# Kernel optimization log

Measured on AMD Instinct MI355X. Metric: run time of the kernel, lower is better.

Reference implementation:

```python
import jax, jax.numpy as jnp
import numpy as np
import math

N_ENTITIES = 200000
N_ITEMS = 100000
N_REL = 40
DIM = 64
N_HEADS = 2
DK = DIM // N_HEADS
N_EDGES = 1500000
K_EDGES = 256
K_ITEMS = 100


def setup_inputs() -> dict:
    key = jax.random.key(0)
    k1, k2, k3, k4, k5, k6 = jax.random.split(key, 6)
    entity_emb = jax.random.normal(k1, (N_ENTITIES, DIM), jnp.float32) * 0.1
    W_Q = jax.random.normal(k2, (DIM, DIM), jnp.float32) * (1.0 / math.sqrt(DIM))
    relation_emb = jax.random.normal(k3, (N_REL - 1, DIM), jnp.float32) * 0.1
    edge_index = jax.random.randint(k4, (2, N_EDGES), 0, N_ENTITIES, jnp.int32)
    # edge_type in [1, N_REL-1]: code indexes relation_emb[edge_type - 1]
    edge_type = jax.random.randint(k5, (N_EDGES,), 1, N_REL, jnp.int32)
    # uniform(0,1) driving the gumbel noise -log(-log(u)); clipped away from 0
    noise_u = jax.random.uniform(k6, (N_EDGES,), jnp.float32, 1e-9, 1.0)
    return {"entity_emb": entity_emb, "W_Q": W_Q, "relation_emb": relation_emb,
            "noise_u": noise_u, "edge_index": edge_index, "edge_type": edge_type}


def reference(entity_emb, W_Q, relation_emb, noise_u, edge_index, edge_type):
    head, tail = edge_index[0], edge_index[1]
    E = edge_index.shape[1]

    # --- norm_attn_computer (AttnHGCN): per-edge multi-head attention ---
    # project once on nodes, then gather (same math as (emb[head] @ W_Q))
    proj = entity_emb @ W_Q                               # [N, D]
    q = proj[head].reshape(E, N_HEADS, DK)                # [E, H, Dk]
    k = proj[tail].reshape(E, N_HEADS, DK)                # [E, H, Dk]
    rel = relation_emb[edge_type - 1].reshape(E, N_HEADS, DK)
    attn = jnp.sum(q * k * rel, axis=-1) / math.sqrt(DK)  # [E, H]
    edge_attn_logits = attn.mean(axis=-1)                 # [E]

    # scatter_softmax over head nodes, then multiply by head degree (norm)
    seg_max = jax.lax.stop_gradient(
        jax.ops.segment_max(edge_attn_logits, head, num_segments=N_ENTITIES))
    ex = jnp.exp(edge_attn_logits - seg_max[head])
    denom = jax.ops.segment_sum(ex, head, num_segments=N_ENTITIES)
    edge_attn_score = ex / denom[head]
    deg = jax.ops.segment_sum(jnp.ones_like(edge_attn_logits), head,
                              num_segments=N_ENTITIES)
    edge_attn_score = edge_attn_score * deg[head]         # [E]

    # --- attn logit sums per item (head + tail scatter_sum), topk 100 ---
    sum_by_node = (jax.ops.segment_sum(edge_attn_logits, head, num_segments=N_ENTITIES)
                   + jax.ops.segment_sum(edge_attn_logits, tail, num_segments=N_ENTITIES))
    top_items_v, top_attn_items = jax.lax.top_k(sum_by_node[:N_ITEMS], K_ITEMS)

    # --- gumbel-noise injection + edge topk 256 ---
    noisy_score = edge_attn_score + (-jnp.log(-jnp.log(noise_u)))
    topk_v, topk_attn_edge_id = jax.lax.top_k(noisy_score, K_EDGES)

    return (edge_attn_score, topk_v, topk_attn_edge_id, top_items_v, top_attn_items)
```

## Files before the change

### kernel.cpp

```cpp
#include <hip/hip_runtime.h>

#define N_ENTITIES 200000
#define N_ITEMS    100000
#define DIM        64
#define N_EDGES    1500000
#define K_EDGES    256
#define K_ITEMS    100
#define SCALE      0.08838834764831845f

#define CAND_CAP   8192
#define NSCANB     ((N_ENTITIES + 255) / 256)
#define NXCD       8
#define NBLK3      1024

typedef unsigned long long u64;


__device__ __forceinline__ void l2_atomic_add_f32(float* p, float v) {
    asm volatile("global_atomic_add_f32 %0, %1, off" :: "v"(p), "v"(v) : "memory");
}
__device__ __forceinline__ unsigned xcd_atomic_add(unsigned* p, unsigned v) {
    return __hip_atomic_fetch_add(p, v, __ATOMIC_RELAXED, __HIP_MEMORY_SCOPE_WORKGROUP);
}

__device__ __forceinline__ unsigned fkey(float x) {
    unsigned u = __float_as_uint(x);
    return (u & 0x80000000u) ? ~u : (u | 0x80000000u);
}
__device__ __forceinline__ float funkey(unsigned k) {
    return (k & 0x80000000u) ? __uint_as_float(k & 0x7fffffffu)
                             : __uint_as_float(~k);
}

__device__ __forceinline__ unsigned select_digit(const unsigned* __restrict__ hist,
                                                 unsigned Keff, unsigned* above) {
    unsigned cum = 0;
    int b = 255;
    for (; b > 0; --b) {
        unsigned hb = hist[b];
        if (cum + hb >= Keff) break;
        cum += hb;
    }
    *above = cum;
    return (unsigned)b;
}

__global__ __launch_bounds__(256) void proj_kernel(const float* __restrict__ emb,
                                                   const float* __restrict__ W,
                                                   float* __restrict__ proj,
                                                   const int* __restrict__ head,
                                                   unsigned* __restrict__ degiX,
                                                   unsigned* __restrict__ rank) {
    unsigned xcd;
    asm volatile("s_getreg_b32 %0, hwreg(HW_REG_XCC_ID)" : "=s"(xcd));
    xcd &= (NXCD - 1);

    int e = blockIdx.x * blockDim.x + threadIdx.x;
    unsigned rk = 0;
    bool haveEdge = (e < N_EDGES);
    if (haveEdge)
        rk = (xcd << 28) | xcd_atomic_add(&degiX[(size_t)xcd * N_ENTITIES + head[e]], 1u);

    __shared__ float part[4][16][64];
    const int t = threadIdx.x;
    const int c = t & 63;
    const int q = __builtin_amdgcn_readfirstlane(t >> 6);

    float Wreg[16];
#pragma unroll
    for (int j = 0; j < 16; ++j) Wreg[j] = W[(q * 16 + j) * 64 + c];

    const int base = blockIdx.x * 16;
    const float* erow = emb + (size_t)base * 64 + q * 16;

    float acc[16];
#pragma unroll
    for (int r = 0; r < 16; ++r) acc[r] = 0.f;
#pragma unroll
    for (int r = 0; r < 16; ++r) {
#pragma unroll
        for (int j = 0; j < 16; ++j)
            acc[r] += erow[r * 64 + j] * Wreg[j];
    }
#pragma unroll
    for (int r = 0; r < 16; ++r) part[q][r][c] = acc[r];
    __syncthreads();
#pragma unroll
    for (int it = 0; it < 4; ++it) {
        int oi = t + it * 256;
        int r = oi >> 6, cc = oi & 63;
        float s = part[0][r][cc] + part[1][r][cc] + part[2][r][cc] + part[3][r][cc];
        proj[(size_t)(base + r) * 64 + cc] = s;
    }
    if (haveEdge) rank[e] = rk;
}

__global__ void scan1_kernel(unsigned* __restrict__ degiX,
                             unsigned* __restrict__ degtot,
                             unsigned* __restrict__ start,
                             unsigned* __restrict__ bsum) {
    __shared__ unsigned s[256];
    int t = threadIdx.x, i = blockIdx.x * 256 + t;
    unsigned tot = 0;
    if (i < N_ENTITIES) {
        unsigned px[NXCD];
#pragma unroll
        for (int x = 0; x < NXCD; ++x) {
            px[x] = tot;
            tot += degiX[(size_t)x * N_ENTITIES + i];
        }
#pragma unroll
        for (int x = 0; x < NXCD; ++x)
            degiX[(size_t)x * N_ENTITIES + i] = px[x];
        degtot[i] = tot;
    }
    s[t] = tot;
    __syncthreads();
    for (int off = 1; off < 256; off <<= 1) {
        unsigned x = s[t];
        unsigned y = (t >= off) ? s[t - off] : 0u;
        __syncthreads();
        s[t] = x + y;
        __syncthreads();
    }
    if (i < N_ENTITIES) start[i] = s[t] - tot;
    if (t == 255) bsum[blockIdx.x] = s[t];
}

__global__ __launch_bounds__(256) void scan23_kernel(const unsigned* __restrict__ bsum,
                                                     unsigned* __restrict__ start,
                                                     unsigned* __restrict__ degiX) {
    __shared__ unsigned part[4];
    const int b = blockIdx.x;
    const int t = threadIdx.x;
    unsigned s = 0;
    for (int j = t; j < b; j += 256) s += bsum[j];
#pragma unroll
    for (int off = 1; off < 64; off <<= 1) s += __shfl_xor(s, off, 64);
    if ((t & 63) == 0) part[t >> 6] = s;
    __syncthreads();
    unsigned prefix = part[0] + part[1] + part[2] + part[3];
    int i = b * 256 + t;
    if (i < N_ENTITIES) {
        unsigned sg = start[i] + prefix;
        start[i] = sg;
#pragma unroll
        for (int x = 0; x < NXCD; ++x)
            degiX[(size_t)x * N_ENTITIES + i] += sg;
    }
}

__global__ void scatter_kernel(const int* __restrict__ head, const int* __restrict__ tail,
                               const int* __restrict__ etype,
                               unsigned* __restrict__ rank,
                               const unsigned* __restrict__ startX,
                               u64* __restrict__ rec, int csrMode) {
    int i = blockIdx.x * blockDim.x + threadIdx.x;
    if (i >= N_EDGES) return;
    unsigned r = rank[i];
    unsigned x = r >> 28;
    unsigned slot = startX[(size_t)x * N_ENTITIES + head[i]] + (r & 0x0FFFFFFFu);
    u64 R = ((u64)(unsigned)tail[i] << 27) | ((u64)(unsigned)(etype[i] - 1) << 21) | (u64)(unsigned)i;
    rec[slot] = R;
    if (csrMode) rank[i] = slot;
}

__global__ __launch_bounds__(256) void node_pass(const float4* __restrict__ proj4,
                                                 const float4* __restrict__ rel4,
                                                 const u64* __restrict__ rec,
                                                 const unsigned* __restrict__ start,
                                                 const unsigned* __restrict__ degtot,
                                                 float* __restrict__ logitsOut,
                                                 int csrMode,
                                                 float2* __restrict__ nd,
                                                 float* __restrict__ sumhead,
                                                 float* __restrict__ sumtailR,
                                                 int repMask) {
    unsigned xcd;
    asm volatile("s_getreg_b32 %0, hwreg(HW_REG_XCC_ID)" : "=s"(xcd));
    float* st = sumtailR + (size_t)(xcd & (unsigned)repMask) * N_ITEMS;
    const bool xcdLocal = (repMask == NXCD - 1);

    int wave = (blockIdx.x * blockDim.x + threadIdx.x) >> 6;
    int lane = threadIdx.x & 63;
    int slot = lane >> 4, sl = lane & 15;
    unsigned s = start[wave], len = degtot[wave];
    float4 ph = proj4[(size_t)wave * 16 + sl];
    float dsum = 0.f, lsum = 0.f;
    for (unsigned k0 = 0; k0 < len; k0 += 8) {
        unsigned ka = k0 + slot, kb = ka + 4;
        bool va = (ka < len), vb = (kb < len);
        u64 Ra = rec[s + (va ? ka : 0u)];
        u64 Rb = rec[s + (vb ? kb : 0u)];
        unsigned ta = (unsigned)(Ra >> 27), ria = ((unsigned)(Ra >> 21)) & 63u;
        unsigned tb = (unsigned)(Rb >> 27), rib = ((unsigned)(Rb >> 21)) & 63u;
        unsigned ea = (unsigned)Ra & 0x1FFFFFu, eb = (unsigned)Rb & 0x1FFFFFu;
        float4 pa = proj4[(size_t)ta * 16 + sl];
        float4 qa = rel4[(size_t)ria * 16 + sl];
        float4 pb = proj4[(size_t)tb * 16 + sl];
        float4 qb = rel4[(size_t)rib * 16 + sl];
        float xa = ph.x * pa.x * qa.x + ph.y * pa.y * qa.y + ph.z * pa.z * qa.z + ph.w * pa.w * qa.w;
        float xb = ph.x * pb.x * qb.x + ph.y * pb.y * qb.y + ph.z * pb.z * qb.z + ph.w * pb.w * qb.w;
        xa += __shfl_xor(xa, 1, 64);  xb += __shfl_xor(xb, 1, 64);
        xa += __shfl_xor(xa, 2, 64);  xb += __shfl_xor(xb, 2, 64);
        xa += __shfl_xor(xa, 4, 64);  xb += __shfl_xor(xb, 4, 64);
        xa += __shfl_xor(xa, 8, 64);  xb += __shfl_xor(xb, 8, 64);
        if (sl == 0) {
            if (va) {
                float lg = xa * SCALE;
                logitsOut[csrMode ? (s + ka) : ea] = lg;
                dsum += __expf(lg);
                lsum += lg;
                if (ta < N_ITEMS) {
                    if (xcdLocal) l2_atomic_add_f32(&st[ta], lg);
                    else          atomicAdd(&st[ta], lg);
                }
            }
            if (vb) {
                float lg = xb * SCALE;
                logitsOut[csrMode ? (s + kb) : eb] = lg;
                dsum += __expf(lg);
                lsum += lg;
                if (tb < N_ITEMS) {
                    if (xcdLocal) l2_atomic_add_f32(&st[tb], lg);
                    else          atomicAdd(&st[tb], lg);
                }
            }
        }
    }
    dsum += __shfl_xor(dsum, 16, 64);
    dsum += __shfl_xor(dsum, 32, 64);
    lsum += __shfl_xor(lsum, 16, 64);
    lsum += __shfl_xor(lsum, 32, 64);
    if (lane == 0) {
        nd[wave] = make_float2(dsum, (float)len);
        sumhead[wave] = lsum;
    }
}

__global__ __launch_bounds__(256) void edge_pass3(const float* __restrict__ logitsEdge,
                           const float* __restrict__ logitsCsr,
                           const unsigned* __restrict__ slotmap, int csrMode,
                           const int* __restrict__ head,
                           const float2* __restrict__ nd, const float* __restrict__ noise_u,
                           const float* __restrict__ sumhead, const float* __restrict__ sumtailR,
                           int R,
                           float* __restrict__ out_scores, unsigned* __restrict__ keysE,
                           unsigned* __restrict__ keysI, unsigned* __restrict__ histB) {
    __shared__ unsigned hh[512];
    for (int j = threadIdx.x; j < 512; j += blockDim.x) hh[j] = 0;
    __syncthreads();

    const int stride = NBLK3 * 256;
    for (int i = blockIdx.x * blockDim.x + threadIdx.x; i < N_EDGES; i += stride) {
        float lg = csrMode ? logitsCsr[slotmap[i]] : logitsEdge[i];
        float2 dd = nd[head[i]];
        float score = __expf(lg) / dd.x * dd.y;
        out_scores[i] = score;
        float noise = -logf(-logf(noise_u[i]));
        unsigned k = fkey(score + noise);
        keysE[i] = k;
        atomicAdd(&hh[k >> 24], 1u);
        if (i < N_ITEMS) {
            float s = sumhead[i];
            for (int r = 0; r < R; ++r) s += sumtailR[(size_t)r * N_ITEMS + i];
            unsigned ki = fkey(s);
            keysI[i] = ki;
            atomicAdd(&hh[256 + (ki >> 24)], 1u);
        }
    }
    __syncthreads();
    unsigned* row = histB + (size_t)blockIdx.x * 512;
    for (int j = threadIdx.x; j < 512; j += blockDim.x) row[j] = hh[j];
}

__global__ void reduce_hist_kernel(const unsigned* __restrict__ histB,
                                   unsigned* __restrict__ hists) {
    const int bin = blockIdx.x;
    unsigned s = 0;
    for (int r = threadIdx.x; r < NBLK3; r += 64)
        s += histB[(size_t)r * 512 + bin];
#pragma unroll
    for (int off = 1; off < 64; off <<= 1) s += __shfl_xor(s, off, 64);
    if (threadIdx.x == 0) hists[bin] = s;
}

__global__ void collect_kernel(const unsigned* __restrict__ keysE,
                               const unsigned* __restrict__ keysI,
                               const unsigned* __restrict__ hists,
                               unsigned* __restrict__ counters, unsigned* __restrict__ cand) {
    const int y = blockIdx.y;
    const unsigned* keys = y ? keysI : keysE;
    const int n = y ? N_ITEMS : N_EDGES;
    const unsigned K = y ? K_ITEMS : K_EDGES;
    const unsigned* H = hists + (size_t)y * 256;
    unsigned aboveA;
    unsigned binA = select_digit(H, K, &aboveA);
    const unsigned T = binA << 24;
    unsigned* cd = cand + (size_t)y * 2 * CAND_CAP;

    int i = blockIdx.x * blockDim.x + threadIdx.x;
    int stride = gridDim.x * blockDim.x;
    for (; i < n; i += stride) {
        unsigned k = keys[i];
        if (k >= T) {
            unsigned p = atomicAdd(&counters[y], 1u);
            if (p < (unsigned)CAND_CAP) { cd[2 * p] = k; cd[2 * p + 1] = (unsigned)i; }
        }
    }
}

__global__ void final_topk_kernel(const unsigned* __restrict__ cand,
                                  const unsigned* __restrict__ counters,
                                  float* __restrict__ out_topkv, float* __restrict__ out_topki,
                                  float* __restrict__ out_itemv, float* __restrict__ out_itemi) {
    __shared__ unsigned sk[CAND_CAP];
    __shared__ unsigned si[CAND_CAP];
    const int y = blockIdx.x;
    const int K = y ? K_ITEMS : K_EDGES;
    float* outv = y ? out_itemv : out_topkv;
    float* outi = y ? out_itemi : out_topki;
    const unsigned* cd = cand + (size_t)y * 2 * CAND_CAP;
    unsigned m = counters[y];
    if (m > (unsigned)CAND_CAP) m = CAND_CAP;
    for (unsigned i = threadIdx.x; i < m; i += blockDim.x) {
        sk[i] = cd[2 * i];
        si[i] = cd[2 * i + 1];
    }
    __syncthreads();
    for (unsigned i = threadIdx.x; i < m; i += blockDim.x) {
        unsigned ki = sk[i], xi = si[i];
        int r = 0;
        for (unsigned j = 0; j < m; ++j) {
            unsigned kj = sk[j];
            if (kj > ki || (kj == ki && si[j] < xi)) r++;
        }
        if (r < K) {
            outv[r] = funkey(ki);
            outi[r] = (float)xi;
        }
    }
}

extern "C" void kernel_launch(void* const* d_in, const int* in_sizes, int n_in,
                              void* d_out, int out_size, void* d_ws, size_t ws_size,
                              hipStream_t stream) {
    (void)in_sizes; (void)n_in; (void)out_size;
    const float* emb    = (const float*)d_in[0];
    const float* W      = (const float*)d_in[1];
    const float* rel    = (const float*)d_in[2];
    const float* noise  = (const float*)d_in[3];
    const int*   eidx   = (const int*)d_in[4];
    const int*   etype  = (const int*)d_in[5];
    const int* head = eidx;
    const int* tail = eidx + N_EDGES;

    float* out        = (float*)d_out;
    float* out_scores = out;
    float* out_topkv  = out + N_EDGES;
    float* out_topki  = out + N_EDGES + K_EDGES;
    float* out_itemv  = out + N_EDGES + 2 * K_EDGES;
    float* out_itemi  = out + N_EDGES + 2 * K_EDGES + K_ITEMS;

    auto layout_floats = [](int R, int csr) -> size_t {
        return (size_t)N_ENTITIES * DIM + N_EDGES + 2 * (size_t)N_EDGES
             + N_ENTITIES + N_ENTITIES + (size_t)NXCD * N_ENTITIES
             + (size_t)R * N_ITEMS + 2
             + (size_t)NBLK3 * 512 + 512
             + 2 * (size_t)N_ENTITIES + N_ENTITIES
             + 1024 + 2 * 2 * CAND_CAP + (csr ? (size_t)N_EDGES : 0);
    };
    int R = 8, csr = 1;
    while (R > 1 && ws_size < layout_floats(R, 1) * 4) R >>= 1;
    if (ws_size < layout_floats(1, 1) * 4) {
        csr = 0;
        R = 8;
        while (R > 1 && ws_size < layout_floats(R, 0) * 4) R >>= 1;
    }

    float* ws = (float*)d_ws;
    size_t o = 0;
    float*    proj    = ws + o;               o += (size_t)N_ENTITIES * DIM;
    unsigned* rank    = (unsigned*)(ws + o);
    float*    logits  = ws + o;               o += N_EDGES;
    u64*      rec     = (u64*)(ws + o);       o += 2 * (size_t)N_EDGES;
    unsigned* keysE   = (unsigned*)rec;
    unsigned* keysI   = keysE + N_EDGES;
    unsigned* start   = (unsigned*)(ws + o);  o += N_ENTITIES;
    unsigned* degtot  = (unsigned*)(ws + o);  o += N_ENTITIES;
    unsigned* degiX   = (unsigned*)(ws + o);  o += (size_t)NXCD * N_ENTITIES;
    float*    sumtailR= ws + o;               o += (size_t)R * N_ITEMS;
    unsigned* counters= (unsigned*)(ws + o);  o += 2;
    unsigned* histB   = (unsigned*)(ws + o);  o += (size_t)NBLK3 * 512;
    unsigned* hists   = (unsigned*)(ws + o);  o += 512;
    float2*   nd      = (float2*)(ws + o);    o += 2 * (size_t)N_ENTITIES;
    float*    sumhead = ws + o;               o += N_ENTITIES;
    unsigned* bsum    = (unsigned*)(ws + o);  o += 1024;
    unsigned* cand    = (unsigned*)(ws + o);  o += 2 * 2 * CAND_CAP;
    float*    logitsCsr = ws + o;             if (csr) o += N_EDGES;

    float*    nodePassLogits = csr ? logitsCsr : logits;

    hipMemsetAsync(degiX, 0,
                   ((size_t)NXCD * N_ENTITIES + (size_t)R * N_ITEMS + 2) * 4, stream);
    hipLaunchKernelGGL(proj_kernel, dim3(12500), dim3(256), 0, stream,
                       emb, W, proj, head, degiX, rank);
    hipLaunchKernelGGL(scan1_kernel, dim3(NSCANB), dim3(256), 0, stream,
                       degiX, degtot, start, bsum);
    hipLaunchKernelGGL(scan23_kernel, dim3(NSCANB), dim3(256), 0, stream,
                       bsum, start, degiX);
    hipLaunchKernelGGL(scatter_kernel, dim3((N_EDGES + 255) / 256), dim3(256), 0, stream,
                       head, tail, etype, rank, degiX, rec, csr);
    hipLaunchKernelGGL(node_pass, dim3(N_ENTITIES / 4), dim3(256), 0, stream,
                       (const float4*)proj, (const float4*)rel, rec, start, degtot,
                       nodePassLogits, csr, nd, sumhead, sumtailR, R - 1);
    hipLaunchKernelGGL(edge_pass3, dim3(NBLK3), dim3(256), 0, stream,
                       logits, logitsCsr, rank, csr, head, (const float2*)nd, noise,
                       sumhead, sumtailR, R,
                       out_scores, keysE, keysI, histB);
    hipLaunchKernelGGL(reduce_hist_kernel, dim3(512), dim3(64), 0, stream, histB, hists);
    hipLaunchKernelGGL(collect_kernel, dim3(512, 2), dim3(256), 0, stream,
                       keysE, keysI, hists, counters, cand);
    hipLaunchKernelGGL(final_topk_kernel, dim3(2), dim3(1024), 0, stream,
                       cand, counters, out_topkv, out_topki, out_itemv, out_itemi);
}
```

Measured before the change: 465.1 us.

## Replace CSR build and node pass with edge-parallel atomic accumulation

```diff
diff --git a/kernel.cpp b/kernel.cpp
--- a/kernel.cpp
+++ b/kernel.cpp
@@ -9,19 +9,10 @@
 #define SCALE      0.08838834764831845f
 
 #define CAND_CAP   8192
-#define NSCANB     ((N_ENTITIES + 255) / 256)
-#define NXCD       8
 #define NBLK3      1024
 
 typedef unsigned long long u64;
 
-
-__device__ __forceinline__ void l2_atomic_add_f32(float* p, float v) {
-    asm volatile("global_atomic_add_f32 %0, %1, off" :: "v"(p), "v"(v) : "memory");
-}
-__device__ __forceinline__ unsigned xcd_atomic_add(unsigned* p, unsigned v) {
-    return __hip_atomic_fetch_add(p, v, __ATOMIC_RELAXED, __HIP_MEMORY_SCOPE_WORKGROUP);
-}
 
 __device__ __forceinline__ unsigned fkey(float x) {
     unsigned u = __float_as_uint(x);
@@ -49,17 +40,9 @@
                                                    const float* __restrict__ W,
                                                    float* __restrict__ proj,
                                                    const int* __restrict__ head,
-                                                   unsigned* __restrict__ degiX,
-                                                   unsigned* __restrict__ rank) {
-    unsigned xcd;
-    asm volatile("s_getreg_b32 %0, hwreg(HW_REG_XCC_ID)" : "=s"(xcd));
-    xcd &= (NXCD - 1);
-
+                                                   float* __restrict__ ndf) {
     int e = blockIdx.x * blockDim.x + threadIdx.x;
-    unsigned rk = 0;
-    bool haveEdge = (e < N_EDGES);
-    if (haveEdge)
-        rk = (xcd << 28) | xcd_atomic_add(&degiX[(size_t)xcd * N_ENTITIES + head[e]], 1u);
+    if (e < N_EDGES) atomicAdd(&ndf[2 * head[e] + 1], 1.0f);
 
     __shared__ float part[4][16][64];
     const int t = threadIdx.x;
@@ -92,159 +75,58 @@
         float s = part[0][r][cc] + part[1][r][cc] + part[2][r][cc] + part[3][r][cc];
         proj[(size_t)(base + r) * 64 + cc] = s;
     }
-    if (haveEdge) rank[e] = rk;
-}
-
-__global__ void scan1_kernel(unsigned* __restrict__ degiX,
-                             unsigned* __restrict__ degtot,
-                             unsigned* __restrict__ start,
-                             unsigned* __restrict__ bsum) {
-    __shared__ unsigned s[256];
-    int t = threadIdx.x, i = blockIdx.x * 256 + t;
-    unsigned tot = 0;
-    if (i < N_ENTITIES) {
-        unsigned px[NXCD];
-#pragma unroll
-        for (int x = 0; x < NXCD; ++x) {
-            px[x] = tot;
-            tot += degiX[(size_t)x * N_ENTITIES + i];
-        }
-#pragma unroll
-        for (int x = 0; x < NXCD; ++x)
-            degiX[(size_t)x * N_ENTITIES + i] = px[x];
-        degtot[i] = tot;
-    }
-    s[t] = tot;
-    __syncthreads();
-    for (int off = 1; off < 256; off <<= 1) {
-        unsigned x = s[t];
-        unsigned y = (t >= off) ? s[t - off] : 0u;
-        __syncthreads();
-        s[t] = x + y;
-        __syncthreads();
-    }
-    if (i < N_ENTITIES) start[i] = s[t] - tot;
-    if (t == 255) bsum[blockIdx.x] = s[t];
-}
-
-__global__ __launch_bounds__(256) void scan23_kernel(const unsigned* __restrict__ bsum,
-                                                     unsigned* __restrict__ start,
-                                                     unsigned* __restrict__ degiX) {
-    __shared__ unsigned part[4];
-    const int b = blockIdx.x;
-    const int t = threadIdx.x;
-    unsigned s = 0;
-    for (int j = t; j < b; j += 256) s += bsum[j];
-#pragma unroll
-    for (int off = 1; off < 64; off <<= 1) s += __shfl_xor(s, off, 64);
-    if ((t & 63) == 0) part[t >> 6] = s;
-    __syncthreads();
-    unsigned prefix = part[0] + part[1] + part[2] + part[3];
-    int i = b * 256 + t;
-    if (i < N_ENTITIES) {
-        unsigned sg = start[i] + prefix;
-        start[i] = sg;
-#pragma unroll
-        for (int x = 0; x < NXCD; ++x)
-            degiX[(size_t)x * N_ENTITIES + i] += sg;
-    }
-}
-
-__global__ void scatter_kernel(const int* __restrict__ head, const int* __restrict__ tail,
-                               const int* __restrict__ etype,
-                               unsigned* __restrict__ rank,
-                               const unsigned* __restrict__ startX,
-                               u64* __restrict__ rec, int csrMode) {
-    int i = blockIdx.x * blockDim.x + threadIdx.x;
-    if (i >= N_EDGES) return;
-    unsigned r = rank[i];
-    unsigned x = r >> 28;
-    unsigned slot = startX[(size_t)x * N_ENTITIES + head[i]] + (r & 0x0FFFFFFFu);
-    u64 R = ((u64)(unsigned)tail[i] << 27) | ((u64)(unsigned)(etype[i] - 1) << 21) | (u64)(unsigned)i;
-    rec[slot] = R;
-    if (csrMode) rank[i] = slot;
-}
-
-__global__ __launch_bounds__(256) void node_pass(const float4* __restrict__ proj4,
+}
+
+__global__ __launch_bounds__(256) void edge_main(const float4* __restrict__ proj4,
                                                  const float4* __restrict__ rel4,
-                                                 const u64* __restrict__ rec,
-                                                 const unsigned* __restrict__ start,
-                                                 const unsigned* __restrict__ degtot,
-                                                 float* __restrict__ logitsOut,
-                                                 int csrMode,
-                                                 float2* __restrict__ nd,
-                                                 float* __restrict__ sumhead,
-                                                 float* __restrict__ sumtailR,
-                                                 int repMask) {
-    unsigned xcd;
-    asm volatile("s_getreg_b32 %0, hwreg(HW_REG_XCC_ID)" : "=s"(xcd));
-    float* st = sumtailR + (size_t)(xcd & (unsigned)repMask) * N_ITEMS;
-    const bool xcdLocal = (repMask == NXCD - 1);
-
+                                                 const int* __restrict__ head,
+                                                 const int* __restrict__ tail,
+                                                 const int* __restrict__ etype,
+                                                 float* __restrict__ logits,
+                                                 float* __restrict__ ndf,
+                                                 float* __restrict__ sumI) {
     int wave = (blockIdx.x * blockDim.x + threadIdx.x) >> 6;
     int lane = threadIdx.x & 63;
     int slot = lane >> 4, sl = lane & 15;
-    unsigned s = start[wave], len = degtot[wave];
-    float4 ph = proj4[(size_t)wave * 16 + sl];
-    float dsum = 0.f, lsum = 0.f;
-    for (unsigned k0 = 0; k0 < len; k0 += 8) {
-        unsigned ka = k0 + slot, kb = ka + 4;
-        bool va = (ka < len), vb = (kb < len);
-        u64 Ra = rec[s + (va ? ka : 0u)];
-        u64 Rb = rec[s + (vb ? kb : 0u)];
-        unsigned ta = (unsigned)(Ra >> 27), ria = ((unsigned)(Ra >> 21)) & 63u;
-        unsigned tb = (unsigned)(Rb >> 27), rib = ((unsigned)(Rb >> 21)) & 63u;
-        unsigned ea = (unsigned)Ra & 0x1FFFFFu, eb = (unsigned)Rb & 0x1FFFFFu;
-        float4 pa = proj4[(size_t)ta * 16 + sl];
-        float4 qa = rel4[(size_t)ria * 16 + sl];
-        float4 pb = proj4[(size_t)tb * 16 + sl];
-        float4 qb = rel4[(size_t)rib * 16 + sl];
-        float xa = ph.x * pa.x * qa.x + ph.y * pa.y * qa.y + ph.z * pa.z * qa.z + ph.w * pa.w * qa.w;
-        float xb = ph.x * pb.x * qb.x + ph.y * pb.y * qb.y + ph.z * pb.z * qb.z + ph.w * pb.w * qb.w;
-        xa += __shfl_xor(xa, 1, 64);  xb += __shfl_xor(xb, 1, 64);
-        xa += __shfl_xor(xa, 2, 64);  xb += __shfl_xor(xb, 2, 64);
-        xa += __shfl_xor(xa, 4, 64);  xb += __shfl_xor(xb, 4, 64);
-        xa += __shfl_xor(xa, 8, 64);  xb += __shfl_xor(xb, 8, 64);
-        if (sl == 0) {
-            if (va) {
-                float lg = xa * SCALE;
-                logitsOut[csrMode ? (s + ka) : ea] = lg;
-                dsum += __expf(lg);
-                lsum += lg;
-                if (ta < N_ITEMS) {
-                    if (xcdLocal) l2_atomic_add_f32(&st[ta], lg);
-                    else          atomicAdd(&st[ta], lg);
-                }
-            }
-            if (vb) {
-                float lg = xb * SCALE;
-                logitsOut[csrMode ? (s + kb) : eb] = lg;
-                dsum += __expf(lg);
-                lsum += lg;
-                if (tb < N_ITEMS) {
-                    if (xcdLocal) l2_atomic_add_f32(&st[tb], lg);
-                    else          atomicAdd(&st[tb], lg);
-                }
-            }
-        }
-    }
-    dsum += __shfl_xor(dsum, 16, 64);
-    dsum += __shfl_xor(dsum, 32, 64);
-    lsum += __shfl_xor(lsum, 16, 64);
-    lsum += __shfl_xor(lsum, 32, 64);
-    if (lane == 0) {
-        nd[wave] = make_float2(dsum, (float)len);
-        sumhead[wave] = lsum;
-    }
-}
-
-__global__ __launch_bounds__(256) void edge_pass3(const float* __restrict__ logitsEdge,
-                           const float* __restrict__ logitsCsr,
-                           const unsigned* __restrict__ slotmap, int csrMode,
+    int ea = wave * 8 + slot, eb = ea + 4;
+
+    int ha  = head[ea],  hb  = head[eb];
+    int tta = tail[ea],  ttb = tail[eb];
+    int ria = etype[ea] - 1, rib = etype[eb] - 1;
+
+    float4 pha = proj4[(size_t)ha  * 16 + sl];
+    float4 pta = proj4[(size_t)tta * 16 + sl];
+    float4 qra = rel4[(size_t)ria * 16 + sl];
+    float4 phb = proj4[(size_t)hb  * 16 + sl];
+    float4 ptb = proj4[(size_t)ttb * 16 + sl];
+    float4 qrb = rel4[(size_t)rib * 16 + sl];
+
+    float xa = pha.x * pta.x * qra.x + pha.y * pta.y * qra.y
+             + pha.z * pta.z * qra.z + pha.w * pta.w * qra.w;
+    float xb = phb.x * ptb.x * qrb.x + phb.y * ptb.y * qrb.y
+             + phb.z * ptb.z * qrb.z + phb.w * ptb.w * qrb.w;
+    xa += __shfl_xor(xa, 1, 64);  xb += __shfl_xor(xb, 1, 64);
+    xa += __shfl_xor(xa, 2, 64);  xb += __shfl_xor(xb, 2, 64);
+    xa += __shfl_xor(xa, 4, 64);  xb += __shfl_xor(xb, 4, 64);
+    xa += __shfl_xor(xa, 8, 64);  xb += __shfl_xor(xb, 8, 64);
+
+    if (sl == 0) {
+        float lga = xa * SCALE, lgb = xb * SCALE;
+        logits[ea] = lga;
+        logits[eb] = lgb;
+        atomicAdd(&ndf[2 * ha], __expf(lga));
+        atomicAdd(&ndf[2 * hb], __expf(lgb));
+        if (ha  < N_ITEMS) atomicAdd(&sumI[ha],  lga);
+        if (tta < N_ITEMS) atomicAdd(&sumI[tta], lga);
+        if (hb  < N_ITEMS) atomicAdd(&sumI[hb],  lgb);
+        if (ttb < N_ITEMS) atomicAdd(&sumI[ttb], lgb);
+    }
+}
+
+__global__ __launch_bounds__(256) void edge_pass3(const float* __restrict__ logits,
                            const int* __restrict__ head,
-                           const float2* __restrict__ nd, const float* __restrict__ noise_u,
-                           const float* __restrict__ sumhead, const float* __restrict__ sumtailR,
-                           int R,
+                           const float* __restrict__ ndf, const float* __restrict__ noise_u,
+                           const float* __restrict__ sumI,
                            float* __restrict__ out_scores, unsigned* __restrict__ keysE,
                            unsigned* __restrict__ keysI, unsigned* __restrict__ histB) {
     __shared__ unsigned hh[512];
@@ -253,8 +135,8 @@
 
     const int stride = NBLK3 * 256;
     for (int i = blockIdx.x * blockDim.x + threadIdx.x; i < N_EDGES; i += stride) {
-        float lg = csrMode ? logitsCsr[slotmap[i]] : logitsEdge[i];
-        float2 dd = nd[head[i]];
+        float lg = logits[i];
+        float2 dd = ((const float2*)ndf)[head[i]];
         float score = __expf(lg) / dd.x * dd.y;
         out_scores[i] = score;
         float noise = -logf(-logf(noise_u[i]));
@@ -262,9 +144,7 @@
         keysE[i] = k;
         atomicAdd(&hh[k >> 24], 1u);
         if (i < N_ITEMS) {
-            float s = sumhead[i];
-            for (int r = 0; r < R; ++r) s += sumtailR[(size_t)r * N_ITEMS + i];
-            unsigned ki = fkey(s);
+            unsigned ki = fkey(sumI[i]);
             keysI[i] = ki;
             atomicAdd(&hh[256 + (ki >> 24)], 1u);
         }
@@ -345,7 +225,7 @@
 extern "C" void kernel_launch(void* const* d_in, const int* in_sizes, int n_in,
                               void* d_out, int out_size, void* d_ws, size_t ws_size,
                               hipStream_t stream) {
-    (void)in_sizes; (void)n_in; (void)out_size;
+    (void)in_sizes; (void)n_in; (void)out_size; (void)ws_size;
     const float* emb    = (const float*)d_in[0];
     const float* W      = (const float*)d_in[1];
     const float* rel    = (const float*)d_in[2];
@@ -362,61 +242,27 @@
     float* out_itemv  = out + N_EDGES + 2 * K_EDGES;
     float* out_itemi  = out + N_EDGES + 2 * K_EDGES + K_ITEMS;
 
-    auto layout_floats = [](int R, int csr) -> size_t {
-        return (size_t)N_ENTITIES * DIM + N_EDGES + 2 * (size_t)N_EDGES
-             + N_ENTITIES + N_ENTITIES + (size_t)NXCD * N_ENTITIES
-             + (size_t)R * N_ITEMS + 2
-             + (size_t)NBLK3 * 512 + 512
-             + 2 * (size_t)N_ENTITIES + N_ENTITIES
-             + 1024 + 2 * 2 * CAND_CAP + (csr ? (size_t)N_EDGES : 0);
-    };
-    int R = 8, csr = 1;
-    while (R > 1 && ws_size < layout_floats(R, 1) * 4) R >>= 1;
-    if (ws_size < layout_floats(1, 1) * 4) {
-        csr = 0;
-        R = 8;
-        while (R > 1 && ws_size < layout_floats(R, 0) * 4) R >>= 1;
-    }
-
     float* ws = (float*)d_ws;
     size_t o = 0;
     float*    proj    = ws + o;               o += (size_t)N_ENTITIES * DIM;
-    unsigned* rank    = (unsigned*)(ws + o);
+    float*    ndf     = ws + o;               o += 2 * (size_t)N_ENTITIES;
+    float*    sumI    = ws + o;               o += N_ITEMS;
+    unsigned* counters= (unsigned*)(ws + o);  o += 2;
     float*    logits  = ws + o;               o += N_EDGES;
-    u64*      rec     = (u64*)(ws + o);       o += 2 * (size_t)N_EDGES;
-    unsigned* keysE   = (unsigned*)rec;
-    unsigned* keysI   = keysE + N_EDGES;
-    unsigned* start   = (unsigned*)(ws + o);  o += N_ENTITIES;
-    unsigned* degtot  = (unsigned*)(ws + o);  o += N_ENTITIES;
-    unsigned* degiX   = (unsigned*)(ws + o);  o += (size_t)NXCD * N_ENTITIES;
-    float*    sumtailR= ws + o;               o += (size_t)R * N_ITEMS;
-    unsigned* counters= (unsigned*)(ws + o);  o += 2;
+    unsigned* keysE   = (unsigned*)(ws + o);  o += N_EDGES;
+    unsigned* keysI   = (unsigned*)(ws + o);  o += N_ITEMS;
     unsigned* histB   = (unsigned*)(ws + o);  o += (size_t)NBLK3 * 512;
     unsigned* hists   = (unsigned*)(ws + o);  o += 512;
-    float2*   nd      = (float2*)(ws + o);    o += 2 * (size_t)N_ENTITIES;
-    float*    sumhead = ws + o;               o += N_ENTITIES;
-    unsigned* bsum    = (unsigned*)(ws + o);  o += 1024;
     unsigned* cand    = (unsigned*)(ws + o);  o += 2 * 2 * CAND_CAP;
-    float*    logitsCsr = ws + o;             if (csr) o += N_EDGES;
-
-    float*    nodePassLogits = csr ? logitsCsr : logits;
-
-    hipMemsetAsync(degiX, 0,
-                   ((size_t)NXCD * N_ENTITIES + (size_t)R * N_ITEMS + 2) * 4, stream);
+
+    hipMemsetAsync(ndf, 0, (2 * (size_t)N_ENTITIES + N_ITEMS + 2) * 4, stream);
     hipLaunchKernelGGL(proj_kernel, dim3(12500), dim3(256), 0, stream,
-                       emb, W, proj, head, degiX, rank);
-    hipLaunchKernelGGL(scan1_kernel, dim3(NSCANB), dim3(256), 0, stream,
-                       degiX, degtot, start, bsum);
-    hipLaunchKernelGGL(scan23_kernel, dim3(NSCANB), dim3(256), 0, stream,
-                       bsum, start, degiX);
-    hipLaunchKernelGGL(scatter_kernel, dim3((N_EDGES + 255) / 256), dim3(256), 0, stream,
-                       head, tail, etype, rank, degiX, rec, csr);
-    hipLaunchKernelGGL(node_pass, dim3(N_ENTITIES / 4), dim3(256), 0, stream,
-                       (const float4*)proj, (const float4*)rel, rec, start, degtot,
-                       nodePassLogits, csr, nd, sumhead, sumtailR, R - 1);
+                       emb, W, proj, head, ndf);
+    hipLaunchKernelGGL(edge_main, dim3(46875), dim3(256), 0, stream,
+                       (const float4*)proj, (const float4*)rel, head, tail, etype,
+                       logits, ndf, sumI);
     hipLaunchKernelGGL(edge_pass3, dim3(NBLK3), dim3(256), 0, stream,
-                       logits, logitsCsr, rank, csr, head, (const float2*)nd, noise,
-                       sumhead, sumtailR, R,
+                       logits, head, ndf, noise, sumI,
                        out_scores, keysE, keysI, histB);
     hipLaunchKernelGGL(reduce_hist_kernel, dim3(512), dim3(64), 0, stream, histB, hists);
     hipLaunchKernelGGL(collect_kernel, dim3(512, 2), dim3(256), 0, stream,
```

Result: slower. 476.1 us (+2.4%).
